# Performance work log

Hardware: AMD Instinct MI355X
Metric: run time of the kernel (lower is better)

## Reference

```python
import jax, jax.numpy as jnp
import numpy as np

N_NODES = 100000
FEAT_DIM = 256
EMBED_DIM = 256
BATCH = 50000
NUM_SAMPLE = 16


def setup_inputs() -> dict:
    key = jax.random.key(0)
    k1, k2, k3, k4 = jax.random.split(key, 4)
    nodes = jax.random.randint(k1, (BATCH,), 0, N_NODES, dtype=jnp.int64 if jax.config.jax_enable_x64 else jnp.int32)
    neigh_idx = jax.random.randint(k2, (BATCH, NUM_SAMPLE), 0, N_NODES, dtype=nodes.dtype)
    features = jax.random.normal(k3, (N_NODES, FEAT_DIM), dtype=jnp.float32)
    # xavier-uniform-like init for weight [embed_dim, 2*feat_dim]
    fan_in, fan_out = 2 * FEAT_DIM, EMBED_DIM
    limit = float(np.sqrt(6.0 / (fan_in + fan_out)))
    weight = jax.random.uniform(k4, (EMBED_DIM, 2 * FEAT_DIM), dtype=jnp.float32, minval=-limit, maxval=limit)
    return {"nodes": nodes, "neigh_idx": neigh_idx, "features": features, "weight": weight}


def reference(nodes, neigh_idx, features, weight) -> jnp.ndarray:
    # Mean aggregator over sampled neighbors: [B, S, F] -> [B, F]
    neigh_feats = jnp.mean(features[neigh_idx], axis=1)
    # Self embedding lookup: [B, F]
    self_feats = features[nodes]
    # combined: [B, 2F]
    combined = jnp.concatenate([self_feats, neigh_feats], axis=1)
    # kernel == 'GCN' path: relu(W @ combined.T) -> [embed_dim, B]
    out = jax.nn.relu(jnp.einsum("ef,bf->eb", weight, combined))
    return out
```

## Files before the change

kernel.cpp:

```cpp
#include <hip/hip_runtime.h>

#define N_NODES 100000
#define B_TOTAL 50000
#define NSAMP   16
#define FDIM    256
#define KDIM    512
#define EDIM    256
#define NBT     64
#define B_PAD   50048
#define NBLK    (B_PAD / NBT)

#define XCHUNK  16384
#define XBLK    (4 * XCHUNK)
#define WIMG_OFF ((size_t)NBLK * XBLK)
#define WIMG_SZ  (4 * 65536)
#define F8_OFF   (WIMG_OFF + WIMG_SZ)
#define F8_SZ    ((size_t)N_NODES * FDIM)

typedef __attribute__((ext_vector_type(4))) float float4v;
typedef __attribute__((ext_vector_type(2))) float float2v;
typedef __attribute__((ext_vector_type(4))) short short4v;
typedef __attribute__((ext_vector_type(8))) short short8v;
typedef __attribute__((ext_vector_type(2))) unsigned int uint2v;

__device__ __forceinline__ unsigned short f2bf(float f) {
  unsigned int u = __builtin_bit_cast(unsigned int, f);
  u += 0x7FFFu + ((u >> 16) & 1u);
  return (unsigned short)(u >> 16);
}

__device__ __forceinline__ short4v pack4(float4v v) {
  short4v r;
  r[0] = (short)f2bf(v[0]);
  r[1] = (short)f2bf(v[1]);
  r[2] = (short)f2bf(v[2]);
  r[3] = (short)f2bf(v[3]);
  return r;
}

#if defined(__has_builtin)
#if __has_builtin(__builtin_amdgcn_cvt_pk_f32_fp8) && __has_builtin(__builtin_amdgcn_cvt_pk_fp8_f32)
#define HAS_HW_FP8 1
#endif
#endif

#ifdef HAS_HW_FP8
__device__ __forceinline__ float2v f8_lo(unsigned int d) {
  return (float2v)__builtin_amdgcn_cvt_pk_f32_fp8((int)d, false);
}
__device__ __forceinline__ float2v f8_hi(unsigned int d) {
  return (float2v)__builtin_amdgcn_cvt_pk_f32_fp8((int)d, true);
}
__device__ __forceinline__ uint2v f8_enc8(float4v a, float4v b) {
  int w0 = __builtin_amdgcn_cvt_pk_fp8_f32(a[0], a[1], 0, false);
  w0 = __builtin_amdgcn_cvt_pk_fp8_f32(a[2], a[3], w0, true);
  int w1 = __builtin_amdgcn_cvt_pk_fp8_f32(b[0], b[1], 0, false);
  w1 = __builtin_amdgcn_cvt_pk_fp8_f32(b[2], b[3], w1, true);
  uint2v r; r[0] = (unsigned)w0; r[1] = (unsigned)w1;
  return r;
}
#else
__device__ __forceinline__ float f8_dec1(unsigned int b) {
  unsigned int s = b >> 7, e = (b >> 3) & 15, m = b & 7;
  float fn = __builtin_bit_cast(float, (s << 31) | ((e + 120) << 23) | (m << 20));
  float fs = (float)(int)m * 0.001953125f;
  fs = s ? -fs : fs;
  return e ? fn : fs;
}
__device__ __forceinline__ float2v f8_lo(unsigned int d) {
  float2v r; r[0] = f8_dec1(d & 255u); r[1] = f8_dec1((d >> 8) & 255u); return r;
}
__device__ __forceinline__ float2v f8_hi(unsigned int d) {
  float2v r; r[0] = f8_dec1((d >> 16) & 255u); r[1] = f8_dec1(d >> 24); return r;
}
__device__ __forceinline__ unsigned int f8_enc1(float x) {
  unsigned int u = __builtin_bit_cast(unsigned int, x);
  unsigned int s = (u >> 31) << 7;
  float ax = __builtin_fabsf(x);
  if (ax < 0.015625f) {
    unsigned int m = (unsigned int)__builtin_rintf(ax * 512.0f);
    return s | m;
  }
  if (ax > 448.0f) return s | 0x7E;
  unsigned int au = u & 0x7fffffffu;
  unsigned int t = au + 0x7FFFFu + ((au >> 20) & 1u);
  unsigned int E = t >> 23;
  return s | (((E - 120u) & 0xFu) << 3) | ((t >> 20) & 7u);
}
__device__ __forceinline__ uint2v f8_enc8(float4v a, float4v b) {
  uint2v r;
  r[0] = f8_enc1(a[0]) | (f8_enc1(a[1]) << 8) | (f8_enc1(a[2]) << 16) | (f8_enc1(a[3]) << 24);
  r[1] = f8_enc1(b[0]) | (f8_enc1(b[1]) << 8) | (f8_enc1(b[2]) << 16) | (f8_enc1(b[3]) << 24);
  return r;
}
#endif

__device__ __forceinline__ unsigned int ld4(const void* p) {
  unsigned int r;
  asm volatile("global_load_dword %0, %1, off" : "=v"(r) : "v"(p) : "memory");
  return r;
}
__device__ __forceinline__ float4v ld16f(const void* p) {
  float4v r;
  asm volatile("global_load_dwordx4 %0, %1, off" : "=v"(r) : "v"(p) : "memory");
  return r;
}

__device__ __forceinline__ void lds_load16(const void* g, void* l) {
  __builtin_amdgcn_global_load_lds(
      (const __attribute__((address_space(1))) unsigned int*)g,
      (__attribute__((address_space(3))) unsigned int*)l, 16, 0, 0);
}

__global__ __launch_bounds__(256) void fp8_pack(
    const float* __restrict__ f, unsigned char* __restrict__ o) {
  const size_t i = ((size_t)blockIdx.x * 256 + threadIdx.x) * 8;
  if (i >= (size_t)N_NODES * FDIM) return;
  float4v a = *(const float4v*)(f + i);
  float4v b = *(const float4v*)(f + i + 4);
  *(uint2v*)(o + i) = f8_enc8(a, b);
}

__global__ __launch_bounds__(256) void pack_w(
    const float* __restrict__ weight, unsigned char* __restrict__ wimg) {
  const int idx = blockIdx.x * 256 + threadIdx.x;
  const int e  = idx >> 7;
  const int kq = idx & 127;
  const int k  = kq * 4;
  const int kc = k >> 7;
  const int kl = k & 127;
  float4v wv = *(const float4v*)(weight + (size_t)e * KDIM + k);
  *(short4v*)(wimg + kc * 65536 + e * 256 +
              (((unsigned)(kl * 2)) ^ ((unsigned)(e & 7) << 4))) = pack4(wv);
}

__global__ __launch_bounds__(256, 4) void gather_mean_f8(
    const int* __restrict__ nodes,
    const int* __restrict__ neigh,
    const float* __restrict__ features,
    const unsigned char* __restrict__ f8,
    unsigned char* __restrict__ ximg) {
  const int l = threadIdx.x & 63;
  const int w = threadIdx.x >> 6;
  const int row = __builtin_amdgcn_readfirstlane(blockIdx.x * 4 + w);
  if (row >= B_PAD) return;

  const int blk  = row >> 6;
  const int rloc = row & 63;
  unsigned char* base = ximg + (size_t)blk * XBLK + rloc * 256;
  const unsigned int sw  = (unsigned)(rloc & 7) << 4;
  const unsigned int off = (((unsigned)(l * 8)) & 255u) ^ sw;
  const int kcs = l >> 5;

  if (row < B_TOTAL) {
    const int node = nodes[row];
    const int* ni = neigh + row * NSAMP;
    float4v vs = ld16f(features + (size_t)node * FDIM + l * 4);
    const size_t fo = (size_t)l * 4;
    unsigned int d0  = ld4(f8 + (size_t)ni[ 0] * FDIM + fo);
    unsigned int d1  = ld4(f8 + (size_t)ni[ 1] * FDIM + fo);
    unsigned int d2  = ld4(f8 + (size_t)ni[ 2] * FDIM + fo);
    unsigned int d3  = ld4(f8 + (size_t)ni[ 3] * FDIM + fo);
    unsigned int d4  = ld4(f8 + (size_t)ni[ 4] * FDIM + fo);
    unsigned int d5  = ld4(f8 + (size_t)ni[ 5] * FDIM + fo);
    unsigned int d6  = ld4(f8 + (size_t)ni[ 6] * FDIM + fo);
    unsigned int d7  = ld4(f8 + (size_t)ni[ 7] * FDIM + fo);
    unsigned int d8  = ld4(f8 + (size_t)ni[ 8] * FDIM + fo);
    unsigned int d9  = ld4(f8 + (size_t)ni[ 9] * FDIM + fo);
    unsigned int d10 = ld4(f8 + (size_t)ni[10] * FDIM + fo);
    unsigned int d11 = ld4(f8 + (size_t)ni[11] * FDIM + fo);
    unsigned int d12 = ld4(f8 + (size_t)ni[12] * FDIM + fo);
    unsigned int d13 = ld4(f8 + (size_t)ni[13] * FDIM + fo);
    unsigned int d14 = ld4(f8 + (size_t)ni[14] * FDIM + fo);
    unsigned int d15 = ld4(f8 + (size_t)ni[15] * FDIM + fo);
    asm volatile("s_waitcnt vmcnt(0)" ::: "memory");
    __builtin_amdgcn_sched_barrier(0);

    float2v lo0 = f8_lo(d0)  + f8_lo(d1);
    float2v lo1 = f8_lo(d2)  + f8_lo(d3);
    float2v lo2 = f8_lo(d4)  + f8_lo(d5);
    float2v lo3 = f8_lo(d6)  + f8_lo(d7);
    float2v lo4 = f8_lo(d8)  + f8_lo(d9);
    float2v lo5 = f8_lo(d10) + f8_lo(d11);
    float2v lo6 = f8_lo(d12) + f8_lo(d13);
    float2v lo7 = f8_lo(d14) + f8_lo(d15);
    lo0 += lo1; lo2 += lo3; lo4 += lo5; lo6 += lo7;
    lo0 += lo2; lo4 += lo6;
    lo0 += lo4;
    float2v hi0 = f8_hi(d0)  + f8_hi(d1);
    float2v hi1 = f8_hi(d2)  + f8_hi(d3);
    float2v hi2 = f8_hi(d4)  + f8_hi(d5);
    float2v hi3 = f8_hi(d6)  + f8_hi(d7);
    float2v hi4 = f8_hi(d8)  + f8_hi(d9);
    float2v hi5 = f8_hi(d10) + f8_hi(d11);
    float2v hi6 = f8_hi(d12) + f8_hi(d13);
    float2v hi7 = f8_hi(d14) + f8_hi(d15);
    hi0 += hi1; hi2 += hi3; hi4 += hi5; hi6 += hi7;
    hi0 += hi2; hi4 += hi6;
    hi0 += hi4;

    float4v a0;
    a0[0] = lo0[0] * 0.0625f;
    a0[1] = lo0[1] * 0.0625f;
    a0[2] = hi0[0] * 0.0625f;
    a0[3] = hi0[1] * 0.0625f;

    *(short4v*)(base + kcs * XCHUNK + off)       = pack4(vs);
    *(short4v*)(base + (2 + kcs) * XCHUNK + off) = pack4(a0);
  } else {
    short4v z = {0, 0, 0, 0};
    *(short4v*)(base + kcs * XCHUNK + off)       = z;
    *(short4v*)(base + (2 + kcs) * XCHUNK + off) = z;
  }
}

__global__ __launch_bounds__(256) void gemm_relu(
    const unsigned char* __restrict__ ximg,
    const unsigned char* __restrict__ wimg,
    float* __restrict__ out) {
  __shared__ alignas(16) unsigned char lds_w[EDIM * 256];
  __shared__ alignas(16) unsigned char lds_x[NBT * 256];

  const int tid = threadIdx.x;
  const int l   = tid & 63;
  const int w   = tid >> 6;
  const int lr  = l & 15;
  const int g   = l >> 4;
  const int b0  = blockIdx.x * NBT;
  const unsigned char* xsrc = ximg + (size_t)blockIdx.x * XBLK;

  float4v acc[4][4];
  #pragma unroll
  for (int mi = 0; mi < 4; ++mi)
    #pragma unroll
    for (int ni = 0; ni < 4; ++ni)
      acc[mi][ni] = (float4v){0.f, 0.f, 0.f, 0.f};

  typedef __attribute__((ext_vector_type(8))) short short8vv;
  for (int kc = 0; kc < 4; ++kc) {
    __syncthreads();
    {
      const unsigned char* ws_ = wimg + kc * 65536;
      #pragma unroll
      for (int i = 0; i < 16; ++i)
        lds_load16(ws_ + i * 4096 + tid * 16, lds_w + i * 4096 + (w << 10));
      const unsigned char* xs_ = xsrc + kc * XCHUNK;
      #pragma unroll
      for (int i = 0; i < 4; ++i)
        lds_load16(xs_ + i * 4096 + tid * 16, lds_x + i * 4096 + (w << 10));
    }
    __syncthreads();
    #pragma unroll
    for (int ks = 0; ks < 4; ++ks) {
      const int ko = ks * 32;
      short8vv afr[4], bfr[4];
      #pragma unroll
      for (int mi = 0; mi < 4; ++mi) {
        const int e = w * 64 + mi * 16 + lr;
        const unsigned int sw = (unsigned)(e & 7) << 4;
        const unsigned char* base = lds_w + e * 256;
        short4v lo = *(const short4v*)(base + (((unsigned)((ko + 4 * g) * 2)) ^ sw));
        short4v hi = *(const short4v*)(base + (((unsigned)((ko + 16 + 4 * g) * 2)) ^ sw));
        afr[mi] = __builtin_shufflevector(lo, hi, 0, 1, 2, 3, 4, 5, 6, 7);
      }
      #pragma unroll
      for (int ni = 0; ni < 4; ++ni) {
        const int r = ni * 16 + lr;
        const unsigned int sw = (unsigned)(r & 7) << 4;
        const unsigned char* base = lds_x + r * 256;
        short4v lo = *(const short4v*)(base + (((unsigned)((ko + 4 * g) * 2)) ^ sw));
        short4v hi = *(const short4v*)(base + (((unsigned)((ko + 16 + 4 * g) * 2)) ^ sw));
        bfr[ni] = __builtin_shufflevector(lo, hi, 0, 1, 2, 3, 4, 5, 6, 7);
      }
      #pragma unroll
      for (int mi = 0; mi < 4; ++mi)
        #pragma unroll
        for (int ni = 0; ni < 4; ++ni)
          acc[mi][ni] = __builtin_amdgcn_mfma_f32_16x16x32_bf16(afr[mi], bfr[ni], acc[mi][ni], 0, 0, 0);
    }
  }

  #pragma unroll
  for (int ni = 0; ni < 4; ++ni) {
    const int b = b0 + ni * 16 + lr;
    if (b >= B_TOTAL) continue;
    #pragma unroll
    for (int mi = 0; mi < 4; ++mi) {
      const int e = w * 64 + mi * 16 + g * 4;
      #pragma unroll
      for (int q = 0; q < 4; ++q) {
        float v = acc[mi][ni][q];
        out[(size_t)(e + q) * B_TOTAL + b] = v > 0.f ? v : 0.f;
      }
    }
  }
}

__global__ __launch_bounds__(256, 1) void encoder_fused(
    const int* __restrict__ nodes,
    const int* __restrict__ neigh,
    const float* __restrict__ features,
    const float* __restrict__ weight,
    float* __restrict__ out) {
  __shared__ alignas(16) unsigned char lds_cmb[64 * KDIM * 2];
  __shared__ alignas(16) unsigned char lds_w[EDIM * 128 * 2];

  const int tid = threadIdx.x;
  const int l   = tid & 63;
  const int w   = tid >> 6;
  const int b0  = blockIdx.x * 64;

  for (int rr = 0; rr < 16; ++rr) {
    const int r  = w * 16 + rr;
    const int rb = b0 + r;
    unsigned char* rowp = lds_cmb + r * (KDIM * 2);
    const unsigned int sw = (unsigned)(r & 7) << 4;
    if (rb < B_TOTAL) {
      const int node = nodes[rb];
      float4v selfv = *(const float4v*)(features + (size_t)node * FDIM + l * 4);
      float4v accv = {0.f, 0.f, 0.f, 0.f};
      #pragma unroll
      for (int s = 0; s < NSAMP; ++s) {
        const int ni = neigh[rb * NSAMP + s];
        accv += *(const float4v*)(features + (size_t)ni * FDIM + l * 4);
      }
      accv *= 0.0625f;
      *(short4v*)(rowp + (((unsigned)(l * 8)) ^ sw))       = pack4(selfv);
      *(short4v*)(rowp + (((unsigned)(512 + l * 8)) ^ sw)) = pack4(accv);
    } else {
      short4v z = {0, 0, 0, 0};
      *(short4v*)(rowp + (((unsigned)(l * 8)) ^ sw))       = z;
      *(short4v*)(rowp + (((unsigned)(512 + l * 8)) ^ sw)) = z;
    }
  }

  const int lr = l & 15;
  const int g  = l >> 4;
  float4v acc[4][4];
  #pragma unroll
  for (int mi = 0; mi < 4; ++mi)
    #pragma unroll
    for (int ni = 0; ni < 4; ++ni)
      acc[mi][ni] = (float4v){0.f, 0.f, 0.f, 0.f};

  for (int kc = 0; kc < 4; ++kc) {
    __syncthreads();
    const int k0 = kc * 128;
    for (int i = tid; i < EDIM * 32; i += 256) {
      const int e  = i >> 5;
      const int kq = i & 31;
      float4v wv = *(const float4v*)(weight + (size_t)e * KDIM + k0 + kq * 4);
      *(short4v*)(lds_w + e * 256 + (((unsigned)(kq * 8)) ^ ((unsigned)(e & 7) << 4))) = pack4(wv);
    }
    __syncthreads();
    #pragma unroll
    for (int ks = 0; ks < 4; ++ks) {
      const int ko = ks * 32;
      short8v afr[4], bfr[4];
      #pragma unroll
      for (int mi = 0; mi < 4; ++mi) {
        const int e = w * 64 + mi * 16 + lr;
        const unsigned int sw = (unsigned)(e & 7) << 4;
        const unsigned char* base = lds_w + e * 256;
        short4v lo = *(const short4v*)(base + (((unsigned)((ko + 4 * g) * 2)) ^ sw));
        short4v hi = *(const short4v*)(base + (((unsigned)((ko + 16 + 4 * g) * 2)) ^ sw));
        afr[mi] = __builtin_shufflevector(lo, hi, 0, 1, 2, 3, 4, 5, 6, 7);
      }
      #pragma unroll
      for (int ni = 0; ni < 4; ++ni) {
        const int rrow = ni * 16 + lr;
        const unsigned int sw = (unsigned)(rrow & 7) << 4;
        const unsigned char* base = lds_cmb + rrow * (KDIM * 2);
        const int kk = k0 + ko;
        short4v lo = *(const short4v*)(base + (((unsigned)((kk + 4 * g) * 2)) ^ sw));
        short4v hi = *(const short4v*)(base + (((unsigned)((kk + 16 + 4 * g) * 2)) ^ sw));
        bfr[ni] = __builtin_shufflevector(lo, hi, 0, 1, 2, 3, 4, 5, 6, 7);
      }
      #pragma unroll
      for (int mi = 0; mi < 4; ++mi)
        #pragma unroll
        for (int ni = 0; ni < 4; ++ni)
          acc[mi][ni] = __builtin_amdgcn_mfma_f32_16x16x32_bf16(afr[mi], bfr[ni], acc[mi][ni], 0, 0, 0);
    }
  }

  #pragma unroll
  for (int ni = 0; ni < 4; ++ni) {
    const int b = b0 + ni * 16 + lr;
    if (b >= B_TOTAL) continue;
    #pragma unroll
    for (int mi = 0; mi < 4; ++mi) {
      const int e = w * 64 + mi * 16 + g * 4;
      #pragma unroll
      for (int q = 0; q < 4; ++q) {
        float v = acc[mi][ni][q];
        out[(size_t)(e + q) * B_TOTAL + b] = v > 0.f ? v : 0.f;
      }
    }
  }
}

extern "C" void kernel_launch(void* const* d_in, const int* in_sizes, int n_in,
                              void* d_out, int out_size, void* d_ws, size_t ws_size,
                              hipStream_t stream) {
  const int*   nodes    = (const int*)d_in[0];
  const int*   neigh    = (const int*)d_in[1];
  const float* features = (const float*)d_in[2];
  const float* weight   = (const float*)d_in[3];
  float*       out      = (float*)d_out;

  if (ws_size >= F8_OFF + F8_SZ) {
    unsigned char* ximg = (unsigned char*)d_ws;
    unsigned char* wimg = (unsigned char*)d_ws + WIMG_OFF;
    unsigned char* f8   = (unsigned char*)d_ws + F8_OFF;
    fp8_pack<<<(N_NODES * FDIM / 8 + 255) / 256, 256, 0, stream>>>(features, f8);
    pack_w<<<128, 256, 0, stream>>>(weight, wimg);
    gather_mean_f8<<<B_PAD / 4, 256, 0, stream>>>(nodes, neigh, features, f8, ximg);
    gemm_relu<<<NBLK, 256, 0, stream>>>(ximg, wimg, out);
  } else {
    encoder_fused<<<(B_TOTAL + 63) / 64, 256, 0, stream>>>(nodes, neigh, features, weight, out);
  }
}
```

Before: 93.08 us.

## Halve GEMM K-chunk to 64 and merge fp8/weight pack kernels

The fp8 feature pack and weight pack kernels are merged into one launch, removing one kernel launch. The GEMM K-chunk shrinks from 128 to 64 elements (8 chunks instead of 4), which halves LDS use per block (from 80KB to 40KB) so more blocks can be resident per CU. The gather writes and weight image layout change to match. The cost is twice as many sync/load phases per block.

Measured after the change: 95.41 us. 1.02x slower.

```diff
diff --git a/kernel.cpp b/kernel.cpp
--- a/kernel.cpp
+++ b/kernel.cpp
@@ -10,12 +10,17 @@
 #define B_PAD   50048
 #define NBLK    (B_PAD / NBT)
 
-#define XCHUNK  16384
-#define XBLK    (4 * XCHUNK)
-#define WIMG_OFF ((size_t)NBLK * XBLK)
-#define WIMG_SZ  (4 * 65536)
+#define XCHUNK   8192
+#define XBLK     (8 * XCHUNK)
+#define XIMG_SZ  ((size_t)NBLK * XBLK)
+#define WIMG_OFF XIMG_SZ
+#define WIMG_SZ  ((size_t)8 * 32768)
 #define F8_OFF   (WIMG_OFF + WIMG_SZ)
 #define F8_SZ    ((size_t)N_NODES * FDIM)
+#define WS_MAIN  (F8_OFF + F8_SZ)
+
+#define FP_BLOCKS 12500
+#define PW_BLOCKS 128
 
 typedef __attribute__((ext_vector_type(4))) float float4v;
 typedef __attribute__((ext_vector_type(2))) float float2v;
@@ -112,26 +117,25 @@
       (__attribute__((address_space(3))) unsigned int*)l, 16, 0, 0);
 }
 
-__global__ __launch_bounds__(256) void fp8_pack(
-    const float* __restrict__ f, unsigned char* __restrict__ o) {
-  const size_t i = ((size_t)blockIdx.x * 256 + threadIdx.x) * 8;
-  if (i >= (size_t)N_NODES * FDIM) return;
-  float4v a = *(const float4v*)(f + i);
-  float4v b = *(const float4v*)(f + i + 4);
-  *(uint2v*)(o + i) = f8_enc8(a, b);
-}
-
-__global__ __launch_bounds__(256) void pack_w(
+__global__ __launch_bounds__(256) void prep_pack(
+    const float* __restrict__ f, unsigned char* __restrict__ o8,
     const float* __restrict__ weight, unsigned char* __restrict__ wimg) {
-  const int idx = blockIdx.x * 256 + threadIdx.x;
-  const int e  = idx >> 7;
-  const int kq = idx & 127;
-  const int k  = kq * 4;
-  const int kc = k >> 7;
-  const int kl = k & 127;
-  float4v wv = *(const float4v*)(weight + (size_t)e * KDIM + k);
-  *(short4v*)(wimg + kc * 65536 + e * 256 +
-              (((unsigned)(kl * 2)) ^ ((unsigned)(e & 7) << 4))) = pack4(wv);
+  if (blockIdx.x < FP_BLOCKS) {
+    const size_t i = ((size_t)blockIdx.x * 256 + threadIdx.x) * 8;
+    float4v a = *(const float4v*)(f + i);
+    float4v b = *(const float4v*)(f + i + 4);
+    *(uint2v*)(o8 + i) = f8_enc8(a, b);
+  } else {
+    const int idx = (blockIdx.x - FP_BLOCKS) * 256 + threadIdx.x;
+    const int e  = idx >> 7;
+    const int kq = idx & 127;
+    const int k  = kq * 4;
+    const int kc = k >> 6;
+    const int kl = k & 63;
+    float4v wv = *(const float4v*)(weight + (size_t)e * KDIM + k);
+    *(short4v*)(wimg + kc * 32768 + e * 128 +
+                (((unsigned)(kl * 2)) ^ ((unsigned)(e & 7) << 4))) = pack4(wv);
+  }
 }
 
 __global__ __launch_bounds__(256, 4) void gather_mean_f8(
@@ -147,10 +151,10 @@
 
   const int blk  = row >> 6;
   const int rloc = row & 63;
-  unsigned char* base = ximg + (size_t)blk * XBLK + rloc * 256;
+  unsigned char* base = ximg + (size_t)blk * XBLK + rloc * 128;
   const unsigned int sw  = (unsigned)(rloc & 7) << 4;
-  const unsigned int off = (((unsigned)(l * 8)) & 255u) ^ sw;
-  const int kcs = l >> 5;
+  const unsigned int off = (((unsigned)(l * 8)) & 127u) ^ sw;
+  const int cs = l >> 4;
 
   if (row < B_TOTAL) {
     const int node = nodes[row];
@@ -205,12 +209,12 @@
     a0[2] = hi0[0] * 0.0625f;
     a0[3] = hi0[1] * 0.0625f;
 
-    *(short4v*)(base + kcs * XCHUNK + off)       = pack4(vs);
-    *(short4v*)(base + (2 + kcs) * XCHUNK + off) = pack4(a0);
+    *(short4v*)(base + cs * XCHUNK + off)       = pack4(vs);
+    *(short4v*)(base + (4 + cs) * XCHUNK + off) = pack4(a0);
   } else {
     short4v z = {0, 0, 0, 0};
-    *(short4v*)(base + kcs * XCHUNK + off)       = z;
-    *(short4v*)(base + (2 + kcs) * XCHUNK + off) = z;
+    *(short4v*)(base + cs * XCHUNK + off)       = z;
+    *(short4v*)(base + (4 + cs) * XCHUNK + off) = z;
   }
 }
 
@@ -218,8 +222,8 @@
     const unsigned char* __restrict__ ximg,
     const unsigned char* __restrict__ wimg,
     float* __restrict__ out) {
-  __shared__ alignas(16) unsigned char lds_w[EDIM * 256];
-  __shared__ alignas(16) unsigned char lds_x[NBT * 256];
+  __shared__ alignas(16) unsigned char lds_w[EDIM * 128];
+  __shared__ alignas(16) unsigned char lds_x[NBT * 128];
 
   const int tid = threadIdx.x;
   const int l   = tid & 63;
@@ -236,29 +240,28 @@
     for (int ni = 0; ni < 4; ++ni)
       acc[mi][ni] = (float4v){0.f, 0.f, 0.f, 0.f};
 
-  typedef __attribute__((ext_vector_type(8))) short short8vv;
-  for (int kc = 0; kc < 4; ++kc) {
+  for (int kc = 0; kc < 8; ++kc) {
     __syncthreads();
     {
-      const unsigned char* ws_ = wimg + kc * 65536;
-      #pragma unroll
-      for (int i = 0; i < 16; ++i)
+      const unsigned char* ws_ = wimg + kc * 32768;
+      #pragma unroll
+      for (int i = 0; i < 8; ++i)
         lds_load16(ws_ + i * 4096 + tid * 16, lds_w + i * 4096 + (w << 10));
       const unsigned char* xs_ = xsrc + kc * XCHUNK;
       #pragma unroll
-      for (int i = 0; i < 4; ++i)
+      for (int i = 0; i < 2; ++i)
         lds_load16(xs_ + i * 4096 + tid * 16, lds_x + i * 4096 + (w << 10));
     }
     __syncthreads();
     #pragma unroll
-    for (int ks = 0; ks < 4; ++ks) {
+    for (int ks = 0; ks < 2; ++ks) {
       const int ko = ks * 32;
-      short8vv afr[4], bfr[4];
+      short8v afr[4], bfr[4];
       #pragma unroll
       for (int mi = 0; mi < 4; ++mi) {
         const int e = w * 64 + mi * 16 + lr;
         const unsigned int sw = (unsigned)(e & 7) << 4;
-        const unsigned char* base = lds_w + e * 256;
+        const unsigned char* base = lds_w + e * 128;
         short4v lo = *(const short4v*)(base + (((unsigned)((ko + 4 * g) * 2)) ^ sw));
         short4v hi = *(const short4v*)(base + (((unsigned)((ko + 16 + 4 * g) * 2)) ^ sw));
         afr[mi] = __builtin_shufflevector(lo, hi, 0, 1, 2, 3, 4, 5, 6, 7);
@@ -267,7 +270,7 @@
       for (int ni = 0; ni < 4; ++ni) {
         const int r = ni * 16 + lr;
         const unsigned int sw = (unsigned)(r & 7) << 4;
-        const unsigned char* base = lds_x + r * 256;
+        const unsigned char* base = lds_x + r * 128;
         short4v lo = *(const short4v*)(base + (((unsigned)((ko + 4 * g) * 2)) ^ sw));
         short4v hi = *(const short4v*)(base + (((unsigned)((ko + 16 + 4 * g) * 2)) ^ sw));
         bfr[ni] = __builtin_shufflevector(lo, hi, 0, 1, 2, 3, 4, 5, 6, 7);
@@ -409,12 +412,11 @@
   const float* weight   = (const float*)d_in[3];
   float*       out      = (float*)d_out;
 
-  if (ws_size >= F8_OFF + F8_SZ) {
+  if (ws_size >= WS_MAIN) {
     unsigned char* ximg = (unsigned char*)d_ws;
     unsigned char* wimg = (unsigned char*)d_ws + WIMG_OFF;
     unsigned char* f8   = (unsigned char*)d_ws + F8_OFF;
-    fp8_pack<<<(N_NODES * FDIM / 8 + 255) / 256, 256, 0, stream>>>(features, f8);
-    pack_w<<<128, 256, 0, stream>>>(weight, wimg);
+    prep_pack<<<FP_BLOCKS + PW_BLOCKS, 256, 0, stream>>>(features, f8, weight, wimg);
     gather_mean_f8<<<B_PAD / 4, 256, 0, stream>>>(nodes, neigh, features, f8, ximg);
     gemm_relu<<<NBLK, 256, 0, stream>>>(ximg, wimg, out);
   } else {
```
